# Kernel optimization log

Measured on AMD Instinct MI355X. Metric: run time of the kernel, lower is better.

The kernel has to match this reference:

```python
import jax, jax.numpy as jnp
import numpy as np

B, D, H, W = 16, 512, 64, 64
K = 64  # clusters
EPS = 1e-12  # torch F.normalize eps


def _l2norm(v, axis):
    n = jnp.linalg.norm(v, axis=axis, keepdims=True)
    return v / jnp.maximum(n, EPS)


def setup_inputs() -> dict:
    key = jax.random.key(0)
    k1, k2, k3, k4 = jax.random.split(key, 4)
    x = jax.random.normal(k1, (B, D, H, W), dtype=jnp.float32)
    # conv weight/bias are independent trainable params after init; sample them
    centers = jax.random.uniform(k2, (K, D), dtype=jnp.float32)
    conv_w = 2.0 * 100.0 * centers + 0.01 * jax.random.normal(k3, (K, D), dtype=jnp.float32)
    conv_b = -100.0 * jnp.linalg.norm(centers, axis=1) + 0.01 * jax.random.normal(k4, (K,), dtype=jnp.float32)
    return {"x": x, "conv_w": conv_w, "conv_b": conv_b, "centers": centers}


def reference(x, conv_w, conv_b, centers):
    b = x.shape[0]
    x_flat = x.reshape(b, D, -1)                       # (B, D, N)
    # 1x1 conv == per-location linear over channels
    logits = jnp.einsum('bdn,kd->bkn', x_flat, conv_w) + conv_b[None, :, None]
    w = jax.nn.softmax(logits, axis=1)                 # softmax over clusters
    # vlad[b,k,d] = sum_n w[b,k,n]*(x[b,d,n] - c[k,d])
    #            = (w @ x^T)[b,k,d] - (sum_n w[b,k,n]) * c[k,d]
    wx = jnp.einsum('bkn,bdn->bkd', w, x_flat)         # (B, K, D)
    wsum = jnp.sum(w, axis=-1)                          # (B, K)
    vlad = wx - wsum[:, :, None] * centers[None]        # (B, K, D)
    vlad = _l2norm(vlad, axis=2)                        # intra-normalize
    vlad = vlad.reshape(b, -1)
    vlad = _l2norm(vlad, axis=1)                        # global L2
    return vlad
```

## Files before the change

kernel.cpp:

```cpp
#include <hip/hip_runtime.h>
#include <hip/hip_bf16.h>
#include <math.h>

#define B_ 16
#define D_ 512
#define N_ 4096
#define K_ 64

typedef __attribute__((ext_vector_type(8))) short bfrag;
typedef __attribute__((ext_vector_type(4))) float f32x4;

static __device__ __forceinline__ float bf2f(unsigned short u) {
    return __uint_as_float(((unsigned)u) << 16);
}
static __device__ __forceinline__ unsigned short f2bf(float v) {
    __hip_bfloat16 h = __float2bfloat16(v);
    union { __hip_bfloat16 h; unsigned short u; } cv; cv.h = h; return cv.u;
}
static __device__ __forceinline__ void split3(float v, unsigned short& h,
                                              unsigned short& m, unsigned short& l) {
    h = f2bf(v); float r1 = v - bf2f(h);
    m = f2bf(r1); float r2 = r1 - bf2f(m);
    l = f2bf(r2);
}
static __device__ __forceinline__ void split2(float v, unsigned short& h,
                                              unsigned short& l) {
    h = f2bf(v); l = f2bf(v - bf2f(h));
}
#define MFMA(a, b, c) __builtin_amdgcn_mfma_f32_16x16x32_bf16((a), (b), (c), 0, 0, 0)

__global__ __launch_bounds__(256) void k_logits_softmax(
    const float* __restrict__ x, const float* __restrict__ conv_w,
    const float* __restrict__ conv_b,
    unsigned short* __restrict__ wh, unsigned short* __restrict__ wl)
{
    const int b   = blockIdx.x >> 5;
    const int n0  = (blockIdx.x & 31) * 128;
    const int tid  = threadIdx.x;
    const int w    = tid >> 6;
    const int lane = tid & 63;
    const int q = lane >> 4;
    const int c = lane & 15;
    const int ktb = (w & 1) * 32;
    const int ntb = (w >> 1) * 64;

    __shared__ unsigned short cws[3][64][40];
    __shared__ unsigned short xs[3][128][40];
    __shared__ float redm[2][128];
    __shared__ float reds[2][128];

    f32x4 acc[2][4];
    #pragma unroll
    for (int kt = 0; kt < 2; ++kt)
        #pragma unroll
        for (int nt = 0; nt < 4; ++nt) acc[kt][nt] = (f32x4){0.f, 0.f, 0.f, 0.f};

    const float* xb = x + (size_t)b * D_ * N_ + n0;

    for (int d0 = 0; d0 < D_; d0 += 32) {
        #pragma unroll
        for (int i = 0; i < 2; ++i) {
            const int s  = i * 256 + tid;
            const int k  = s >> 3;
            const int d4 = (s & 7) * 4;
            const float4 v = *(const float4*)&conv_w[k * D_ + d0 + d4];
            const float vv[4] = {v.x, v.y, v.z, v.w};
            unsigned short h[4], m[4], l[4];
            #pragma unroll
            for (int j = 0; j < 4; ++j) split3(vv[j], h[j], m[j], l[j]);
            *(ushort4*)&cws[0][k][d4] = make_ushort4(h[0], h[1], h[2], h[3]);
            *(ushort4*)&cws[1][k][d4] = make_ushort4(m[0], m[1], m[2], m[3]);
            *(ushort4*)&cws[2][k][d4] = make_ushort4(l[0], l[1], l[2], l[3]);
        }
        #pragma unroll
        for (int i = 0; i < 4; ++i) {
            const int s  = i * 256 + tid;
            const int n  = s & 127;
            const int dg = (s >> 7) * 4;
            unsigned short h[4], m[4], l[4];
            #pragma unroll
            for (int r = 0; r < 4; ++r) {
                const float v = xb[(size_t)(d0 + dg + r) * N_ + n];
                split3(v, h[r], m[r], l[r]);
            }
            *(ushort4*)&xs[0][n][dg] = make_ushort4(h[0], h[1], h[2], h[3]);
            *(ushort4*)&xs[1][n][dg] = make_ushort4(m[0], m[1], m[2], m[3]);
            *(ushort4*)&xs[2][n][dg] = make_ushort4(l[0], l[1], l[2], l[3]);
        }
        __syncthreads();

        bfrag af[2][3];
        #pragma unroll
        for (int kt = 0; kt < 2; ++kt)
            #pragma unroll
            for (int lv = 0; lv < 3; ++lv)
                af[kt][lv] = *(const bfrag*)&cws[lv][ktb + kt * 16 + c][q * 8];
        #pragma unroll
        for (int nt = 0; nt < 4; ++nt) {
            bfrag bf[3];
            #pragma unroll
            for (int lv = 0; lv < 3; ++lv)
                bf[lv] = *(const bfrag*)&xs[lv][ntb + nt * 16 + c][q * 8];
            #pragma unroll
            for (int kt = 0; kt < 2; ++kt) {
                f32x4 a = acc[kt][nt];
                a = MFMA(af[kt][0], bf[0], a);
                a = MFMA(af[kt][0], bf[1], a);
                a = MFMA(af[kt][1], bf[0], a);
                a = MFMA(af[kt][1], bf[1], a);
                a = MFMA(af[kt][0], bf[2], a);
                a = MFMA(af[kt][2], bf[0], a);
                acc[kt][nt] = a;
            }
        }
        __syncthreads();
    }

    #pragma unroll
    for (int kt = 0; kt < 2; ++kt) {
        #pragma unroll
        for (int r = 0; r < 4; ++r) {
            const float bias = conv_b[ktb + kt * 16 + q * 4 + r];
            #pragma unroll
            for (int nt = 0; nt < 4; ++nt) acc[kt][nt][r] += bias;
        }
    }
    float mloc[4];
    #pragma unroll
    for (int nt = 0; nt < 4; ++nt) {
        float m = acc[0][nt][0];
        #pragma unroll
        for (int kt = 0; kt < 2; ++kt)
            #pragma unroll
            for (int r = 0; r < 4; ++r) m = fmaxf(m, acc[kt][nt][r]);
        m = fmaxf(m, __shfl_xor(m, 16));
        m = fmaxf(m, __shfl_xor(m, 32));
        mloc[nt] = m;
    }
    if (q == 0)
        #pragma unroll
        for (int nt = 0; nt < 4; ++nt) redm[w & 1][ntb + nt * 16 + c] = mloc[nt];
    __syncthreads();
    float mall[4];
    #pragma unroll
    for (int nt = 0; nt < 4; ++nt)
        mall[nt] = fmaxf(redm[0][ntb + nt * 16 + c], redm[1][ntb + nt * 16 + c]);

    float sloc[4] = {0.f, 0.f, 0.f, 0.f};
    #pragma unroll
    for (int nt = 0; nt < 4; ++nt) {
        #pragma unroll
        for (int kt = 0; kt < 2; ++kt)
            #pragma unroll
            for (int r = 0; r < 4; ++r) {
                const float e = __expf(acc[kt][nt][r] - mall[nt]);
                acc[kt][nt][r] = e;
                sloc[nt] += e;
            }
        sloc[nt] += __shfl_xor(sloc[nt], 16);
        sloc[nt] += __shfl_xor(sloc[nt], 32);
    }
    if (q == 0)
        #pragma unroll
        for (int nt = 0; nt < 4; ++nt) reds[w & 1][ntb + nt * 16 + c] = sloc[nt];
    __syncthreads();

    #pragma unroll
    for (int nt = 0; nt < 4; ++nt) {
        const float inv = 1.0f / (reds[0][ntb + nt * 16 + c] + reds[1][ntb + nt * 16 + c]);
        #pragma unroll
        for (int kt = 0; kt < 2; ++kt)
            #pragma unroll
            for (int r = 0; r < 4; ++r) {
                const float v = acc[kt][nt][r] * inv;
                unsigned short hi, lo;
                split2(v, hi, lo);
                const size_t idx = ((size_t)b * K_ + ktb + kt * 16 + q * 4 + r) * N_
                                 + n0 + ntb + nt * 16 + c;
                wh[idx] = hi;
                wl[idx] = lo;
            }
    }
}

__global__ __launch_bounds__(256) void k_wx(
    const float* __restrict__ x, const unsigned short* __restrict__ wh,
    const unsigned short* __restrict__ wl, float* __restrict__ vlad)
{
    const int nc = blockIdx.x & 7;
    const int dc = (blockIdx.x >> 3) & 3;
    const int b  = blockIdx.x >> 5;
    const int tid  = threadIdx.x;
    const int w    = tid >> 6;
    const int lane = tid & 63;
    const int q = lane >> 4;
    const int c = lane & 15;
    const int ktb = (w & 1) * 32;
    const int dtb = (w >> 1) * 64;

    __shared__ unsigned short ws2[2][64][40];
    __shared__ unsigned short xs2[2][128][40];

    f32x4 acc[2][4];
    #pragma unroll
    for (int kt = 0; kt < 2; ++kt)
        #pragma unroll
        for (int dt = 0; dt < 4; ++dt) acc[kt][dt] = (f32x4){0.f, 0.f, 0.f, 0.f};

    const float* xb = x + (size_t)b * D_ * N_ + (size_t)dc * 128 * N_;
    const unsigned short* whb = wh + (size_t)b * K_ * N_;
    const unsigned short* wlb = wl + (size_t)b * K_ * N_;

    const int nbase = nc * 512;
    for (int n0 = nbase; n0 < nbase + 512; n0 += 32) {
        {
            const int k  = tid >> 2;
            const int ng = (tid & 3) * 8;
            *(uint4*)&ws2[0][k][ng] = *(const uint4*)&whb[(size_t)k * N_ + n0 + ng];
            *(uint4*)&ws2[1][k][ng] = *(const uint4*)&wlb[(size_t)k * N_ + n0 + ng];
        }
        #pragma unroll
        for (int i = 0; i < 4; ++i) {
            const int s  = i * 256 + tid;
            const int d  = s >> 3;
            const int n4 = (s & 7) * 4;
            const float4 v = *(const float4*)&xb[(size_t)d * N_ + n0 + n4];
            const float vv[4] = {v.x, v.y, v.z, v.w};
            unsigned short h[4], l[4];
            #pragma unroll
            for (int j = 0; j < 4; ++j) split2(vv[j], h[j], l[j]);
            *(ushort4*)&xs2[0][d][n4] = make_ushort4(h[0], h[1], h[2], h[3]);
            *(ushort4*)&xs2[1][d][n4] = make_ushort4(l[0], l[1], l[2], l[3]);
        }
        __syncthreads();

        bfrag afh[2], afl[2];
        #pragma unroll
        for (int kt = 0; kt < 2; ++kt) {
            afh[kt] = *(const bfrag*)&ws2[0][ktb + kt * 16 + c][q * 8];
            afl[kt] = *(const bfrag*)&ws2[1][ktb + kt * 16 + c][q * 8];
        }
        #pragma unroll
        for (int dt = 0; dt < 4; ++dt) {
            const bfrag bh = *(const bfrag*)&xs2[0][dtb + dt * 16 + c][q * 8];
            const bfrag bl = *(const bfrag*)&xs2[1][dtb + dt * 16 + c][q * 8];
            #pragma unroll
            for (int kt = 0; kt < 2; ++kt) {
                f32x4 a = acc[kt][dt];
                a = MFMA(afh[kt], bh, a);
                a = MFMA(afh[kt], bl, a);
                a = MFMA(afl[kt], bh, a);
                acc[kt][dt] = a;
            }
        }
        __syncthreads();
    }

    #pragma unroll
    for (int kt = 0; kt < 2; ++kt)
        #pragma unroll
        for (int dt = 0; dt < 4; ++dt)
            #pragma unroll
            for (int r = 0; r < 4; ++r) {
                const int k = ktb + kt * 16 + q * 4 + r;
                const int d = dc * 128 + dtb + dt * 16 + c;
                atomicAdd(&vlad[((size_t)b * K_ + k) * D_ + d], acc[kt][dt][r]);
            }
}

__global__ __launch_bounds__(256) void k_norm(
    const unsigned short* __restrict__ wh, const unsigned short* __restrict__ wl,
    const float* __restrict__ vlad, const float* __restrict__ centers,
    float* __restrict__ out)
{
    const int b = blockIdx.x >> 6;
    const int k = blockIdx.x & 63;
    const int tid = threadIdx.x;

    const unsigned short* whr = wh + ((size_t)b * K_ + k) * N_;
    const unsigned short* wlr = wl + ((size_t)b * K_ + k) * N_;
    float s = 0.f;
    #pragma unroll
    for (int i = 0; i < 2; ++i) {
        const uint4 ah = *(const uint4*)&whr[(i * 256 + tid) * 8];
        const uint4 al = *(const uint4*)&wlr[(i * 256 + tid) * 8];
        const unsigned u[8] = {ah.x, ah.y, ah.z, ah.w, al.x, al.y, al.z, al.w};
        #pragma unroll
        for (int j = 0; j < 8; ++j) {
            s += __uint_as_float(u[j] << 16);
            s += __uint_as_float(u[j] & 0xffff0000u);
        }
    }
    __shared__ float red1[4];
    #pragma unroll
    for (int off = 32; off > 0; off >>= 1) s += __shfl_down(s, off, 64);
    if ((tid & 63) == 0) red1[tid >> 6] = s;
    __syncthreads();
    const float wsum = red1[0] + red1[1] + red1[2] + red1[3];

    const float* vr = vlad + ((size_t)b * K_ + k) * D_;
    const float* cr = centers + k * D_;
    const float v0 = vr[tid]       - wsum * cr[tid];
    const float v1 = vr[tid + 256] - wsum * cr[tid + 256];

    float ss = v0 * v0 + v1 * v1;
    __shared__ float red2[4];
    #pragma unroll
    for (int off = 32; off > 0; off >>= 1) ss += __shfl_down(ss, off, 64);
    if ((tid & 63) == 0) red2[tid >> 6] = ss;
    __syncthreads();
    const float nrm = sqrtf(red2[0] + red2[1] + red2[2] + red2[3]);
    const float scale = 1.0f / (8.0f * fmaxf(nrm, 1e-12f));

    float* outr = out + ((size_t)b * K_ + k) * D_;
    outr[tid]       = v0 * scale;
    outr[tid + 256] = v1 * scale;
}

extern "C" void kernel_launch(void* const* d_in, const int* in_sizes, int n_in,
                              void* d_out, int out_size, void* d_ws, size_t ws_size,
                              hipStream_t stream) {
    const float* x       = (const float*)d_in[0];
    const float* conv_w  = (const float*)d_in[1];
    const float* conv_b  = (const float*)d_in[2];
    const float* centers = (const float*)d_in[3];
    float* out = (float*)d_out;

    char* wsb = (char*)d_ws;
    float* vlad = (float*)wsb;
    unsigned short* wh = (unsigned short*)(wsb + (2u << 20));
    unsigned short* wl = (unsigned short*)(wsb + (10u << 20));

    hipMemsetAsync(vlad, 0, (size_t)B_ * K_ * D_ * sizeof(float), stream);

    k_logits_softmax<<<B_ * 32, 256, 0, stream>>>(x, conv_w, conv_b, wh, wl);
    k_wx<<<B_ * 4 * 8, 256, 0, stream>>>(x, wh, wl, vlad);
    k_norm<<<B_ * K_, 256, 0, stream>>>(wh, wl, vlad, centers, out);
}
```

Before: 237.6 us.

## Register-prefetch next tiles, pre-split conv weights, fuse wsum into softmax

Both GEMM kernels now load the next d/n tile into registers right after the barrier, so global loads overlap the MFMA work on the current tile. The 3-way bf16 split of conv_w moves into a small prep kernel that runs once, instead of being recomputed in every block. The per-cluster weight sums are accumulated during softmax and written with atomics, so k_norm no longer re-reads wh/wl. The cost is more registers per thread and one extra kernel launch, and the atomic accumulation order is nondeterministic.

```diff
diff --git a/kernel.cpp b/kernel.cpp
--- a/kernel.cpp
+++ b/kernel.cpp
@@ -29,10 +29,25 @@
 }
 #define MFMA(a, b, c) __builtin_amdgcn_mfma_f32_16x16x32_bf16((a), (b), (c), 0, 0, 0)
 
+__global__ __launch_bounds__(256) void k_prep(
+    const float* __restrict__ conv_w, unsigned short* __restrict__ cwL)
+{
+    const int i = blockIdx.x * 256 + threadIdx.x;
+    const float4 v = *(const float4*)&conv_w[i * 4];
+    const float vv[4] = {v.x, v.y, v.z, v.w};
+    unsigned short h[4], m[4], l[4];
+    #pragma unroll
+    for (int j = 0; j < 4; ++j) split3(vv[j], h[j], m[j], l[j]);
+    *(ushort4*)&cwL[0 * (K_ * D_) + i * 4] = make_ushort4(h[0], h[1], h[2], h[3]);
+    *(ushort4*)&cwL[1 * (K_ * D_) + i * 4] = make_ushort4(m[0], m[1], m[2], m[3]);
+    *(ushort4*)&cwL[2 * (K_ * D_) + i * 4] = make_ushort4(l[0], l[1], l[2], l[3]);
+}
+
 __global__ __launch_bounds__(256) void k_logits_softmax(
-    const float* __restrict__ x, const float* __restrict__ conv_w,
+    const float* __restrict__ x, const unsigned short* __restrict__ cwL,
     const float* __restrict__ conv_b,
-    unsigned short* __restrict__ wh, unsigned short* __restrict__ wl)
+    unsigned short* __restrict__ wh, unsigned short* __restrict__ wl,
+    float* __restrict__ wsumbuf)
 {
     const int b   = blockIdx.x >> 5;
     const int n0  = (blockIdx.x & 31) * 128;
@@ -57,37 +72,44 @@
 
     const float* xb = x + (size_t)b * D_ * N_ + n0;
 
-    for (int d0 = 0; d0 < D_; d0 += 32) {
-        #pragma unroll
-        for (int i = 0; i < 2; ++i) {
-            const int s  = i * 256 + tid;
-            const int k  = s >> 3;
-            const int d4 = (s & 7) * 4;
-            const float4 v = *(const float4*)&conv_w[k * D_ + d0 + d4];
-            const float vv[4] = {v.x, v.y, v.z, v.w};
+    const int ks = tid >> 2;
+    const int d8 = (tid & 3) * 8;
+    const int xn = tid & 127;
+    const int xd = (tid >> 7) * 4;
+
+    float px[16];
+    uint4 pcw[3];
+
+    auto load_step = [&](int d0) {
+        #pragma unroll
+        for (int lv = 0; lv < 3; ++lv)
+            pcw[lv] = *(const uint4*)&cwL[lv * (K_ * D_) + ks * D_ + d0 + d8];
+        #pragma unroll
+        for (int i = 0; i < 4; ++i)
+            #pragma unroll
+            for (int r = 0; r < 4; ++r)
+                px[i * 4 + r] = xb[(size_t)(d0 + 8 * i + xd + r) * N_ + xn];
+    };
+
+    load_step(0);
+
+    for (int s = 0; s < 16; ++s) {
+        #pragma unroll
+        for (int lv = 0; lv < 3; ++lv)
+            *(uint4*)&cws[lv][ks][d8] = pcw[lv];
+        #pragma unroll
+        for (int i = 0; i < 4; ++i) {
             unsigned short h[4], m[4], l[4];
             #pragma unroll
-            for (int j = 0; j < 4; ++j) split3(vv[j], h[j], m[j], l[j]);
-            *(ushort4*)&cws[0][k][d4] = make_ushort4(h[0], h[1], h[2], h[3]);
-            *(ushort4*)&cws[1][k][d4] = make_ushort4(m[0], m[1], m[2], m[3]);
-            *(ushort4*)&cws[2][k][d4] = make_ushort4(l[0], l[1], l[2], l[3]);
-        }
-        #pragma unroll
-        for (int i = 0; i < 4; ++i) {
-            const int s  = i * 256 + tid;
-            const int n  = s & 127;
-            const int dg = (s >> 7) * 4;
-            unsigned short h[4], m[4], l[4];
-            #pragma unroll
-            for (int r = 0; r < 4; ++r) {
-                const float v = xb[(size_t)(d0 + dg + r) * N_ + n];
-                split3(v, h[r], m[r], l[r]);
-            }
-            *(ushort4*)&xs[0][n][dg] = make_ushort4(h[0], h[1], h[2], h[3]);
-            *(ushort4*)&xs[1][n][dg] = make_ushort4(m[0], m[1], m[2], m[3]);
-            *(ushort4*)&xs[2][n][dg] = make_ushort4(l[0], l[1], l[2], l[3]);
+            for (int r = 0; r < 4; ++r) split3(px[i * 4 + r], h[r], m[r], l[r]);
+            const int dg = 8 * i + xd;
+            *(ushort4*)&xs[0][xn][dg] = make_ushort4(h[0], h[1], h[2], h[3]);
+            *(ushort4*)&xs[1][xn][dg] = make_ushort4(m[0], m[1], m[2], m[3]);
+            *(ushort4*)&xs[2][xn][dg] = make_ushort4(l[0], l[1], l[2], l[3]);
         }
         __syncthreads();
+
+        if (s < 15) load_step((s + 1) * 32);
 
         bfrag af[2][3];
         #pragma unroll
@@ -117,14 +139,14 @@
     }
 
     #pragma unroll
-    for (int kt = 0; kt < 2; ++kt) {
+    for (int kt = 0; kt < 2; ++kt)
         #pragma unroll
         for (int r = 0; r < 4; ++r) {
             const float bias = conv_b[ktb + kt * 16 + q * 4 + r];
             #pragma unroll
             for (int nt = 0; nt < 4; ++nt) acc[kt][nt][r] += bias;
         }
-    }
+
     float mloc[4];
     #pragma unroll
     for (int nt = 0; nt < 4; ++nt) {
@@ -165,6 +187,7 @@
         for (int nt = 0; nt < 4; ++nt) reds[w & 1][ntb + nt * 16 + c] = sloc[nt];
     __syncthreads();
 
+    float wacc[2][4] = {{0.f, 0.f, 0.f, 0.f}, {0.f, 0.f, 0.f, 0.f}};
     #pragma unroll
     for (int nt = 0; nt < 4; ++nt) {
         const float inv = 1.0f / (reds[0][ntb + nt * 16 + c] + reds[1][ntb + nt * 16 + c]);
@@ -179,8 +202,22 @@
                                  + n0 + ntb + nt * 16 + c;
                 wh[idx] = hi;
                 wl[idx] = lo;
-            }
-    }
+                wacc[kt][r] += v;
+            }
+    }
+    #pragma unroll
+    for (int msk = 1; msk < 16; msk <<= 1)
+        #pragma unroll
+        for (int kt = 0; kt < 2; ++kt)
+            #pragma unroll
+            for (int r = 0; r < 4; ++r)
+                wacc[kt][r] += __shfl_xor(wacc[kt][r], msk);
+    if (c == 0)
+        #pragma unroll
+        for (int kt = 0; kt < 2; ++kt)
+            #pragma unroll
+            for (int r = 0; r < 4; ++r)
+                atomicAdd(&wsumbuf[b * K_ + ktb + kt * 16 + q * 4 + r], wacc[kt][r]);
 }
 
 __global__ __launch_bounds__(256) void k_wx(
@@ -211,28 +248,42 @@
     const unsigned short* whb = wh + (size_t)b * K_ * N_;
     const unsigned short* wlb = wl + (size_t)b * K_ * N_;
 
+    const int wk = tid >> 2;
+    const int wn = (tid & 3) * 8;
+    const int xd = tid >> 3;
+    const int xn = (tid & 7) * 4;
+
+    uint4 pw[2];
+    float px[16];
+
+    auto load_step = [&](int n0) {
+        pw[0] = *(const uint4*)&whb[(size_t)wk * N_ + n0 + wn];
+        pw[1] = *(const uint4*)&wlb[(size_t)wk * N_ + n0 + wn];
+        #pragma unroll
+        for (int i = 0; i < 4; ++i) {
+            const float4 v = *(const float4*)&xb[(size_t)(i * 32 + xd) * N_ + n0 + xn];
+            px[i * 4 + 0] = v.x; px[i * 4 + 1] = v.y;
+            px[i * 4 + 2] = v.z; px[i * 4 + 3] = v.w;
+        }
+    };
+
     const int nbase = nc * 512;
-    for (int n0 = nbase; n0 < nbase + 512; n0 += 32) {
-        {
-            const int k  = tid >> 2;
-            const int ng = (tid & 3) * 8;
-            *(uint4*)&ws2[0][k][ng] = *(const uint4*)&whb[(size_t)k * N_ + n0 + ng];
-            *(uint4*)&ws2[1][k][ng] = *(const uint4*)&wlb[(size_t)k * N_ + n0 + ng];
-        }
+    load_step(nbase);
+
+    for (int s = 0; s < 16; ++s) {
+        *(uint4*)&ws2[0][wk][wn] = pw[0];
+        *(uint4*)&ws2[1][wk][wn] = pw[1];
         #pragma unroll
         for (int i = 0; i < 4; ++i) {
-            const int s  = i * 256 + tid;
-            const int d  = s >> 3;
-            const int n4 = (s & 7) * 4;
-            const float4 v = *(const float4*)&xb[(size_t)d * N_ + n0 + n4];
-            const float vv[4] = {v.x, v.y, v.z, v.w};
             unsigned short h[4], l[4];
             #pragma unroll
-            for (int j = 0; j < 4; ++j) split2(vv[j], h[j], l[j]);
-            *(ushort4*)&xs2[0][d][n4] = make_ushort4(h[0], h[1], h[2], h[3]);
-            *(ushort4*)&xs2[1][d][n4] = make_ushort4(l[0], l[1], l[2], l[3]);
+            for (int j = 0; j < 4; ++j) split2(px[i * 4 + j], h[j], l[j]);
+            *(ushort4*)&xs2[0][i * 32 + xd][xn] = make_ushort4(h[0], h[1], h[2], h[3]);
+            *(ushort4*)&xs2[1][i * 32 + xd][xn] = make_ushort4(l[0], l[1], l[2], l[3]);
         }
         __syncthreads();
+
+        if (s < 15) load_step(nbase + (s + 1) * 32);
 
         bfrag afh[2], afl[2];
         #pragma unroll
@@ -269,34 +320,14 @@
 }
 
 __global__ __launch_bounds__(256) void k_norm(
-    const unsigned short* __restrict__ wh, const unsigned short* __restrict__ wl,
-    const float* __restrict__ vlad, const float* __restrict__ centers,
-    float* __restrict__ out)
+    const float* __restrict__ wsumbuf, const float* __restrict__ vlad,
+    const float* __restrict__ centers, float* __restrict__ out)
 {
     const int b = blockIdx.x >> 6;
     const int k = blockIdx.x & 63;
     const int tid = threadIdx.x;
 
-    const unsigned short* whr = wh + ((size_t)b * K_ + k) * N_;
-    const unsigned short* wlr = wl + ((size_t)b * K_ + k) * N_;
-    float s = 0.f;
-    #pragma unroll
-    for (int i = 0; i < 2; ++i) {
-        const uint4 ah = *(const uint4*)&whr[(i * 256 + tid) * 8];
-        const uint4 al = *(const uint4*)&wlr[(i * 256 + tid) * 8];
-        const unsigned u[8] = {ah.x, ah.y, ah.z, ah.w, al.x, al.y, al.z, al.w};
-        #pragma unroll
-        for (int j = 0; j < 8; ++j) {
-            s += __uint_as_float(u[j] << 16);
-            s += __uint_as_float(u[j] & 0xffff0000u);
-        }
-    }
-    __shared__ float red1[4];
-    #pragma unroll
-    for (int off = 32; off > 0; off >>= 1) s += __shfl_down(s, off, 64);
-    if ((tid & 63) == 0) red1[tid >> 6] = s;
-    __syncthreads();
-    const float wsum = red1[0] + red1[1] + red1[2] + red1[3];
+    const float wsum = wsumbuf[b * K_ + k];
 
     const float* vr = vlad + ((size_t)b * K_ + k) * D_;
     const float* cr = centers + k * D_;
@@ -327,13 +358,16 @@
     float* out = (float*)d_out;
 
     char* wsb = (char*)d_ws;
-    float* vlad = (float*)wsb;
-    unsigned short* wh = (unsigned short*)(wsb + (2u << 20));
-    unsigned short* wl = (unsigned short*)(wsb + (10u << 20));
-
-    hipMemsetAsync(vlad, 0, (size_t)B_ * K_ * D_ * sizeof(float), stream);
-
-    k_logits_softmax<<<B_ * 32, 256, 0, stream>>>(x, conv_w, conv_b, wh, wl);
+    float* vlad            = (float*)wsb;
+    float* wsumbuf         = (float*)(wsb + (2u << 20));
+    unsigned short* wh     = (unsigned short*)(wsb + (3u << 20));
+    unsigned short* wl     = (unsigned short*)(wsb + (11u << 20));
+    unsigned short* cwL    = (unsigned short*)(wsb + (19u << 20));
+
+    hipMemsetAsync(vlad, 0, (2u << 20) + 4096, stream);
+
+    k_prep<<<32, 256, 0, stream>>>(conv_w, cwL);
+    k_logits_softmax<<<B_ * 32, 256, 0, stream>>>(x, cwL, conv_b, wh, wl, wsumbuf);
     k_wx<<<B_ * 4 * 8, 256, 0, stream>>>(x, wh, wl, vlad);
-    k_norm<<<B_ * K_, 256, 0, stream>>>(wh, wl, vlad, centers, out);
-}
+    k_norm<<<B_ * K_, 256, 0, stream>>>(wsumbuf, vlad, centers, out);
+}
```

New measurement: 261.2 us. 9.9% more time.
